# Optimization experiments

Measured on AMD Instinct MI355X. Metric: run time of the kernel, lower is better.

The kernel has to match this reference:

```python
import jax, jax.numpy as jnp
import numpy as np

NUM_HEADS = 16
DIM_HEAD = 64
SCALE = DIM_HEAD ** -0.5


def setup_inputs() -> dict:
    key = jax.random.key(0)
    k1, k2, k3 = jax.random.split(key, 3)
    b, s, h = 2, 2048, 1024
    x = jax.random.normal(k1, (b, s, h), dtype=jnp.float32)
    w_qkv = jax.random.normal(k2, (3 * h, h), dtype=jnp.float32) * (h ** -0.5)
    w_out = jax.random.normal(k3, (h, h), dtype=jnp.float32) * (h ** -0.5)
    b_out = jnp.zeros((h,), dtype=jnp.float32)
    return {"x": x, "w_qkv": w_qkv, "w_out": w_out, "b_out": b_out}


def reference(x, w_qkv, w_out, b_out):
    b, s, hid = x.shape
    # qkv projection (no bias): [b, s, 3*hid]
    qkv = jnp.einsum('bsh,oh->bso', x, w_qkv)
    # split order in original rearrange is (qkv, heads, dim_head)
    qkv = qkv.reshape(b, s, 3, NUM_HEADS, DIM_HEAD)
    q = jnp.transpose(qkv[:, :, 0], (0, 2, 1, 3))  # [b, H, s, d]
    k = jnp.transpose(qkv[:, :, 1], (0, 2, 1, 3))
    v = jnp.transpose(qkv[:, :, 2], (0, 2, 1, 3))
    # naive attention: full [b, H, s, s] score matrix, as in the source
    att = jnp.einsum('bhxd,bhyd->bhxy', q, k) * SCALE
    att = jax.nn.softmax(att, axis=-1)
    out = jnp.einsum('bhxy,bhyd->bhxd', att, v)  # [b, H, s, d]
    out = jnp.transpose(out, (0, 2, 1, 3)).reshape(b, s, NUM_HEADS * DIM_HEAD)
    return jnp.einsum('bsi,oi->bso', out, w_out) + b_out
```

## Files before the change

### kernel.cpp

```cpp
#include <hip/hip_runtime.h>
#include <hip/hip_bf16.h>

#define B_ 2
#define S_ 2048
#define HID 1024
#define NH 16
#define DH 64
#define QKV_N (3*HID)
#define M_ROWS (B_*S_)

typedef __attribute__((ext_vector_type(8))) short short8;
typedef __attribute__((ext_vector_type(4))) short short4v;
typedef __attribute__((ext_vector_type(4))) float floatx4;
typedef unsigned int uint;

#define QSCALE 0.18033688f

__device__ __forceinline__ short8 load8(const __hip_bfloat16* p) {
    return *(const short8*)p;
}

#if __has_builtin(__builtin_amdgcn_exp2f)
#define EXP2F(x) __builtin_amdgcn_exp2f(x)
#else
#define EXP2F(x) exp2f(x)
#endif

__device__ __forceinline__ uint pack_bf16_2(float lo, float hi) {
    uint ul = __float_as_uint(lo) + 0x8000u;
    uint uh = __float_as_uint(hi) + 0x8000u;
    return __builtin_amdgcn_perm(uh, ul, 0x07060302);
}
__device__ __forceinline__ uint pack_bf16_2_rtne(float lo, float hi) {
    uint ul = __float_as_uint(lo); ul += 0x7FFFu + ((ul >> 16) & 1u);
    uint uh = __float_as_uint(hi); uh += 0x7FFFu + ((uh >> 16) & 1u);
    return __builtin_amdgcn_perm(uh, ul, 0x07060302);
}

#define ASYNC16(gptr, lptr) \
    __builtin_amdgcn_global_load_lds((const __attribute__((address_space(1))) void*)(gptr), \
                                     (__attribute__((address_space(3))) void*)(lptr), 16, 0, 0)
#define RAW_BARRIER() asm volatile("s_barrier" ::: "memory")

__global__ __launch_bounds__(256) void cvt_all(
    const float* __restrict__ x, const float* __restrict__ wq,
    const float* __restrict__ wo, __hip_bfloat16* __restrict__ out)
{
    const int n0 = M_ROWS * HID, n1 = QKV_N * HID;
    int i = (blockIdx.x * 256 + threadIdx.x) * 4;
    const float* src; int off;
    if (i < n0)           { src = x;  off = i; }
    else if (i < n0 + n1) { src = wq; off = i - n0; }
    else                  { src = wo; off = i - n0 - n1; }
    float4 v = *(const float4*)(src + off);
    uint2 r;
    r.x = pack_bf16_2_rtne(v.x, v.y);
    r.y = pack_bf16_2_rtne(v.z, v.w);
    *(uint2*)(out + i) = r;
}

#define BK 32
#define NITER 32
template<int MODE, int TMB>
__global__ __launch_bounds__(256, (TMB == 128) ? 3 : 4) void gemm_bt_kernel(
    const __hip_bfloat16* __restrict__ A,
    const __hip_bfloat16* __restrict__ Bw,
    const float* __restrict__ biasf,
    __hip_bfloat16* __restrict__ C,
    float* __restrict__ Cf,
    __hip_bfloat16* __restrict__ VT,
    int Mdim, int Ndim, int Kdim)
{
    constexpr int NI = TMB / 32;
    constexpr int CA = TMB / 64;
    constexpr int WAITG = 0x0F70 | (CA + 2);
    __shared__ alignas(16) __hip_bfloat16 As[3][TMB * BK];
    __shared__ alignas(16) __hip_bfloat16 Bs[3][128 * BK];

    const int tid  = threadIdx.x;
    const int wave = tid >> 6;
    const int lane = tid & 63;
    const int q = lane >> 4;
    const int r = lane & 15;
    const int m_blk = blockIdx.y * TMB;
    const int n_blk = blockIdx.x * 128;
    const int wm = (wave >> 1) * (TMB / 2);
    const int wn = (wave & 1) * 64;

    const __hip_bfloat16* Abase = A + (size_t)m_blk * Kdim;
    const __hip_bfloat16* Bbase = Bw + (size_t)n_blk * Kdim;

    floatx4 acc[NI][4];
#pragma unroll
    for (int i = 0; i < NI; i++)
#pragma unroll
        for (int j = 0; j < 4; j++) acc[i][j] = (floatx4){0.f, 0.f, 0.f, 0.f};

    auto stage = [&](int bf, int kt) {
#pragma unroll
        for (int c = 0; c < CA; c++) {
            int ch = tid + c * 256;
            ASYNC16(Abase + (size_t)(ch >> 2) * Kdim + kt + (ch & 3) * 8, &As[bf][ch * 8]);
        }
#pragma unroll
        for (int c = 0; c < 2; c++) {
            int ch = tid + c * 256;
            ASYNC16(Bbase + (size_t)(ch >> 2) * Kdim + kt + (ch & 3) * 8, &Bs[bf][ch * 8]);
        }
    };
    auto compute = [&](int bf) {
        short8 a[NI], b[4];
#pragma unroll
        for (int i = 0; i < NI; i++) a[i] = *(const short8*)&As[bf][(wm + i * 16 + r) * BK + q * 8];
#pragma unroll
        for (int j = 0; j < 4; j++) b[j] = *(const short8*)&Bs[bf][(wn + j * 16 + r) * BK + q * 8];
#pragma unroll
        for (int i = 0; i < NI; i++)
#pragma unroll
            for (int j = 0; j < 4; j++)
                acc[i][j] = __builtin_amdgcn_mfma_f32_16x16x32_bf16(b[j], a[i], acc[i][j], 0, 0, 0);
    };

    stage(0, 0);
    stage(1, BK);
#pragma unroll 3
    for (int it = 0; it < NITER - 2; it++) {
        __builtin_amdgcn_s_waitcnt(WAITG);
        RAW_BARRIER();
        stage((it + 2) % 3, (it + 2) * BK);
        compute(it % 3);
    }
    __builtin_amdgcn_s_waitcnt(WAITG);
    RAW_BARRIER();
    compute((NITER - 2) % 3);
    __builtin_amdgcn_s_waitcnt(0x0F70);
    RAW_BARRIER();
    compute((NITER - 1) % 3);

#pragma unroll
    for (int i = 0; i < NI; i++) {
        const int m = m_blk + wm + i * 16 + r;
#pragma unroll
        for (int j = 0; j < 4; j++) {
            const int n0 = n_blk + wn + j * 16 + q * 4;
            if (MODE == 2) {
                float4 bv = *(const float4*)&biasf[n0];
                float4 ov;
                ov.x = acc[i][j][0] + bv.x;
                ov.y = acc[i][j][1] + bv.y;
                ov.z = acc[i][j][2] + bv.z;
                ov.w = acc[i][j][3] + bv.w;
                *(float4*)&Cf[(size_t)m * Ndim + n0] = ov;
            } else if (n_blk < 2 * HID) {
                float s = (n0 < HID) ? QSCALE : 1.0f;
                uint2 pk;
                pk.x = pack_bf16_2_rtne(acc[i][j][0] * s, acc[i][j][1] * s);
                pk.y = pack_bf16_2_rtne(acc[i][j][2] * s, acc[i][j][3] * s);
                *(uint2*)&C[(size_t)m * QKV_N + n0] = pk;
            } else {
                int bidx = m >> 11;
                int srow = m & (S_ - 1);
                int c = srow & 31;
                int sp = (srow & ~31) | ((c & 15) << 1) | ((c >> 4) & 1);
#pragma unroll
                for (int reg = 0; reg < 4; reg++) {
                    int dfull = n0 + reg - 2 * HID;
                    VT[((size_t)bidx * HID + dfull) * S_ + sp] =
                        __float2bfloat16(acc[i][j][reg]);
                }
            }
        }
    }
}

#define KT 32
#define PPAD 40

__global__ __launch_bounds__(512, 4) void flash_kernel(
    const __hip_bfloat16* __restrict__ qkv,
    const __hip_bfloat16* __restrict__ VTp,
    __hip_bfloat16* __restrict__ O)
{
    __shared__ alignas(16) char smem[69632];
    __hip_bfloat16* lds_k = (__hip_bfloat16*)smem;
    __hip_bfloat16* lds_v = (__hip_bfloat16*)(smem + 24576);
    __hip_bfloat16* lds_p = (__hip_bfloat16*)(smem + 49152);

    const int tid  = threadIdx.x;
    const int wave = tid >> 6;
    const int lane = tid & 63;
    const int q = lane >> 4;
    const int r = lane & 15;
    const int ww   = wave & 3;
    const int khid = wave >> 2;
    const int bh = blockIdx.x;
    const int b  = bh >> 4;
    const int h  = bh & 15;
    const int s0 = blockIdx.y * 128 + ww * 32;

    const __hip_bfloat16* Qbase = qkv + (size_t)b * S_ * QKV_N + h * DH;
    const __hip_bfloat16* Kbase = Qbase + HID;
    const __hip_bfloat16* Vbase = VTp + ((size_t)b * HID + h * DH) * S_;

    const int sr = ww * 8 + (lane >> 3);
    const int kcg = (lane & 7) ^ ((lane >> 3) & 7);
    const __hip_bfloat16* gK = Kbase + (size_t)(khid * 1024 + sr) * QKV_N + kcg * 8;
    const int kldso = sr * 64 + (lane & 7) * 8;
    const int vr = ww * 16 + (lane >> 2);
    const int fv = (vr + (vr >> 2)) & 3;
    const int vcg = (lane & 3) ^ fv;
    const __hip_bfloat16* gV = Vbase + (size_t)vr * S_ + khid * 1024 + vcg * 8;
    const int vldso = vr * 32 + (lane & 3) * 8;

    auto stage = [&](int bf, int it) {
        ASYNC16(gK + (size_t)(it * KT) * QKV_N, &lds_k[(bf * 2 + khid) * 2048 + kldso]);
        ASYNC16(gV + it * KT,                   &lds_v[(bf * 2 + khid) * 2048 + vldso]);
    };

    floatx4 o_acc[2][4];
    floatx4 l_acc[2];
#pragma unroll
    for (int rt = 0; rt < 2; rt++) {
        l_acc[rt] = (floatx4){0.f, 0.f, 0.f, 0.f};
#pragma unroll
        for (int nb = 0; nb < 4; nb++) o_acc[rt][nb] = (floatx4){0.f, 0.f, 0.f, 0.f};
    }
    short8 ones;
#pragma unroll
    for (int i = 0; i < 8; i++) ones[i] = (short)0x3F80;

    __hip_bfloat16* Pw = &lds_p[wave * 1280];

    short8 a_q[2][2];
    auto compute = [&](int bf) {
        const __hip_bfloat16* Kt = &lds_k[(bf * 2 + khid) * 2048];
        const __hip_bfloat16* Vt = &lds_v[(bf * 2 + khid) * 2048];
        short8 bk[2][2];
#pragma unroll
        for (int ct = 0; ct < 2; ct++)
#pragma unroll
            for (int kh = 0; kh < 2; kh++)
                bk[ct][kh] = *(const short8*)&Kt[(ct * 16 + r) * 64 + ((kh * 4 + q) ^ (r & 7)) * 8];
        short8 vb[4];
#pragma unroll
        for (int nb = 0; nb < 4; nb++) {
            int d = nb * 16 + r;
            vb[nb] = *(const short8*)&Vt[d * 32 + ((q ^ ((d + (d >> 2)) & 3)) * 8)];
        }

        short8 pa[2];
#pragma unroll
        for (int rt = 0; rt < 2; rt++) {
            floatx4 sc[2];
#pragma unroll
            for (int ct = 0; ct < 2; ct++) {
                floatx4 z = (floatx4){0.f, 0.f, 0.f, 0.f};
                z = __builtin_amdgcn_mfma_f32_16x16x32_bf16(a_q[rt][0], bk[ct][0], z, 0, 0, 0);
                z = __builtin_amdgcn_mfma_f32_16x16x32_bf16(a_q[rt][1], bk[ct][1], z, 0, 0, 0);
                sc[ct] = z;
            }
#pragma unroll
            for (int reg = 0; reg < 4; reg++) {
                float e0 = EXP2F(sc[0][reg]);
                float e1 = EXP2F(sc[1][reg]);
                *(uint*)&Pw[(rt * 16 + q * 4 + reg) * PPAD + 2 * r] = pack_bf16_2(e0, e1);
            }
            pa[rt] = *(const short8*)&Pw[(rt * 16 + r) * PPAD + q * 8];
        }

        __builtin_amdgcn_s_setprio(1);
#pragma unroll
        for (int rt = 0; rt < 2; rt++) {
            l_acc[rt] = __builtin_amdgcn_mfma_f32_16x16x32_bf16(pa[rt], ones, l_acc[rt], 0, 0, 0);
#pragma unroll
            for (int nb = 0; nb < 4; nb++)
                o_acc[rt][nb] = __builtin_amdgcn_mfma_f32_16x16x32_bf16(pa[rt], vb[nb], o_acc[rt][nb], 0, 0, 0);
        }
        __builtin_amdgcn_s_setprio(0);
    };

    auto step = [&](int it, int bf) {
        __builtin_amdgcn_s_waitcnt(0x0F72);
        RAW_BARRIER();
        stage((bf + 2) % 3, it + 2);
        compute(bf);
    };

    stage(0, 0);
#pragma unroll
    for (int rt = 0; rt < 2; rt++)
#pragma unroll
        for (int kh = 0; kh < 2; kh++)
            a_q[rt][kh] = load8(Qbase + (size_t)(s0 + rt * 16 + r) * QKV_N + kh * 32 + q * 8);
    __builtin_amdgcn_s_waitcnt(0x0F70);
    stage(1, 1);

    for (int itb = 0; itb < 30; itb += 3) {
        step(itb + 0, 0);
        step(itb + 1, 1);
        step(itb + 2, 2);
    }
    __builtin_amdgcn_s_waitcnt(0x0F72);
    RAW_BARRIER();
    compute(0);
    __builtin_amdgcn_s_waitcnt(0x0F70);
    RAW_BARRIER();
    compute(1);

    __syncthreads();
    float* of = (float*)smem;
    float* lf = (float*)(smem + 32768);
    if (khid == 1) {
#pragma unroll
        for (int rt = 0; rt < 2; rt++) {
#pragma unroll
            for (int nb = 0; nb < 4; nb++)
                *(floatx4*)&of[ww * 2048 + (rt * 4 + nb) * 256 + lane * 4] = o_acc[rt][nb];
            *(floatx4*)&lf[ww * 512 + rt * 256 + lane * 4] = l_acc[rt];
        }
    }
    __syncthreads();
    if (khid == 0) {
#pragma unroll
        for (int rt = 0; rt < 2; rt++) {
            l_acc[rt] += *(const floatx4*)&lf[ww * 512 + rt * 256 + lane * 4];
#pragma unroll
            for (int nb = 0; nb < 4; nb++)
                o_acc[rt][nb] += *(const floatx4*)&of[ww * 2048 + (rt * 4 + nb) * 256 + lane * 4];
        }
#pragma unroll
        for (int rt = 0; rt < 2; rt++) {
#pragma unroll
            for (int reg = 0; reg < 4; reg++) {
                float inv = 1.f / l_acc[rt][reg];
                int srow2 = s0 + rt * 16 + q * 4 + reg;
                __hip_bfloat16* Orow = O + ((size_t)b * S_ + srow2) * HID + h * DH;
#pragma unroll
                for (int nb = 0; nb < 4; nb++)
                    Orow[nb * 16 + r] = __float2bfloat16(o_acc[rt][nb][reg] * inv);
            }
        }
    }
}

extern "C" void kernel_launch(void* const* d_in, const int* in_sizes, int n_in,
                              void* d_out, int out_size, void* d_ws, size_t ws_size,
                              hipStream_t stream) {
    const float* x_f     = (const float*)d_in[0];
    const float* w_qkv_f = (const float*)d_in[1];
    const float* w_out_f = (const float*)d_in[2];
    const float* b_out_f = (const float*)d_in[3];
    float* out = (float*)d_out;

    __hip_bfloat16* xb      = (__hip_bfloat16*)d_ws;
    __hip_bfloat16* wqkvb   = xb    + (size_t)M_ROWS * HID;
    __hip_bfloat16* woutb   = wqkvb + (size_t)QKV_N * HID;
    __hip_bfloat16* qkv_ws  = woutb + (size_t)HID * HID;
    __hip_bfloat16* vt_ws   = qkv_ws + (size_t)M_ROWS * QKV_N;
    __hip_bfloat16* attn_ws = vt_ws + (size_t)B_ * HID * S_;

    dim3 blk(256);
    {
        int ntot = M_ROWS * HID + QKV_N * HID + HID * HID;
        cvt_all<<<dim3(ntot / 1024), blk, 0, stream>>>(x_f, w_qkv_f, w_out_f, xb);
    }

    gemm_bt_kernel<1, 128><<<dim3(QKV_N / 128, M_ROWS / 128), blk, 0, stream>>>(
        xb, wqkvb, nullptr, qkv_ws, nullptr, vt_ws, M_ROWS, QKV_N, HID);
    flash_kernel<<<dim3(B_ * NH, S_ / 128), dim3(512), 0, stream>>>(qkv_ws, vt_ws, attn_ws);
    gemm_bt_kernel<2, 64><<<dim3(HID / 128, M_ROWS / 64), blk, 0, stream>>>(
        attn_ws, woutb, b_out_f, nullptr, out, nullptr, M_ROWS, HID, HID);
}
```

Baseline: 181.0 us.

## Keep softmax probabilities in registers by transposing score MFMA, drop LDS round-trip

Swaps the operand order of the QK^T MFMA so each lane's score accumulator already matches the A-operand layout needed for the PV MFMA, packing exp2 results directly into registers instead of writing P to LDS and reading it back. The V transpose layout written by the QKV GEMM drops its row permutation, and V fragments are now gathered as two 4-element LDS reads to match the new k ordering. This removes the per-wave P scratch in LDS (shrinking shared memory) and its store/load latency, at the cost of more, smaller V reads and a layout change that must stay consistent across both kernels.

Measured after the change: 181.0 us. Within noise of the previous version (-0.0%).

```diff
diff --git a/kernel.cpp b/kernel.cpp
--- a/kernel.cpp
+++ b/kernel.cpp
@@ -12,6 +12,7 @@
 typedef __attribute__((ext_vector_type(8))) short short8;
 typedef __attribute__((ext_vector_type(4))) short short4v;
 typedef __attribute__((ext_vector_type(4))) float floatx4;
+typedef __attribute__((ext_vector_type(4))) unsigned int uint4v;
 typedef unsigned int uint;
 
 #define QSCALE 0.18033688f
@@ -160,12 +161,10 @@
             } else {
                 int bidx = m >> 11;
                 int srow = m & (S_ - 1);
-                int c = srow & 31;
-                int sp = (srow & ~31) | ((c & 15) << 1) | ((c >> 4) & 1);
 #pragma unroll
                 for (int reg = 0; reg < 4; reg++) {
                     int dfull = n0 + reg - 2 * HID;
-                    VT[((size_t)bidx * HID + dfull) * S_ + sp] =
+                    VT[((size_t)bidx * HID + dfull) * S_ + srow] =
                         __float2bfloat16(acc[i][j][reg]);
                 }
             }
@@ -174,17 +173,15 @@
 }
 
 #define KT 32
-#define PPAD 40
 
 __global__ __launch_bounds__(512, 4) void flash_kernel(
     const __hip_bfloat16* __restrict__ qkv,
     const __hip_bfloat16* __restrict__ VTp,
     __hip_bfloat16* __restrict__ O)
 {
-    __shared__ alignas(16) char smem[69632];
+    __shared__ alignas(16) char smem[49152];
     __hip_bfloat16* lds_k = (__hip_bfloat16*)smem;
     __hip_bfloat16* lds_v = (__hip_bfloat16*)(smem + 24576);
-    __hip_bfloat16* lds_p = (__hip_bfloat16*)(smem + 49152);
 
     const int tid  = threadIdx.x;
     const int wave = tid >> 6;
@@ -229,8 +226,6 @@
 #pragma unroll
     for (int i = 0; i < 8; i++) ones[i] = (short)0x3F80;
 
-    __hip_bfloat16* Pw = &lds_p[wave * 1280];
-
     short8 a_q[2][2];
     auto compute = [&](int bf) {
         const __hip_bfloat16* Kt = &lds_k[(bf * 2 + khid) * 2048];
@@ -245,38 +240,36 @@
 #pragma unroll
         for (int nb = 0; nb < 4; nb++) {
             int d = nb * 16 + r;
-            vb[nb] = *(const short8*)&Vt[d * 32 + ((q ^ ((d + (d >> 2)) & 3)) * 8)];
-        }
-
-        short8 pa[2];
+            int fvd = (d + (d >> 2)) & 3;
+            short4v lo = *(const short4v*)&Vt[d * 32 + (((q >> 1) ^ fvd) * 8 + (q & 1) * 4)];
+            short4v hi = *(const short4v*)&Vt[d * 32 + ((((q >> 1) + 2) ^ fvd) * 8 + (q & 1) * 4)];
+            vb[nb] = __builtin_shufflevector(lo, hi, 0, 1, 2, 3, 4, 5, 6, 7);
+        }
+
 #pragma unroll
         for (int rt = 0; rt < 2; rt++) {
             floatx4 sc[2];
 #pragma unroll
             for (int ct = 0; ct < 2; ct++) {
                 floatx4 z = (floatx4){0.f, 0.f, 0.f, 0.f};
-                z = __builtin_amdgcn_mfma_f32_16x16x32_bf16(a_q[rt][0], bk[ct][0], z, 0, 0, 0);
-                z = __builtin_amdgcn_mfma_f32_16x16x32_bf16(a_q[rt][1], bk[ct][1], z, 0, 0, 0);
+                z = __builtin_amdgcn_mfma_f32_16x16x32_bf16(bk[ct][0], a_q[rt][0], z, 0, 0, 0);
+                z = __builtin_amdgcn_mfma_f32_16x16x32_bf16(bk[ct][1], a_q[rt][1], z, 0, 0, 0);
                 sc[ct] = z;
             }
-#pragma unroll
-            for (int reg = 0; reg < 4; reg++) {
-                float e0 = EXP2F(sc[0][reg]);
-                float e1 = EXP2F(sc[1][reg]);
-                *(uint*)&Pw[(rt * 16 + q * 4 + reg) * PPAD + 2 * r] = pack_bf16_2(e0, e1);
-            }
-            pa[rt] = *(const short8*)&Pw[(rt * 16 + r) * PPAD + q * 8];
-        }
-
-        __builtin_amdgcn_s_setprio(1);
-#pragma unroll
-        for (int rt = 0; rt < 2; rt++) {
-            l_acc[rt] = __builtin_amdgcn_mfma_f32_16x16x32_bf16(pa[rt], ones, l_acc[rt], 0, 0, 0);
+            uint4v up;
+            up.x = pack_bf16_2(EXP2F(sc[0][0]), EXP2F(sc[0][1]));
+            up.y = pack_bf16_2(EXP2F(sc[0][2]), EXP2F(sc[0][3]));
+            up.z = pack_bf16_2(EXP2F(sc[1][0]), EXP2F(sc[1][1]));
+            up.w = pack_bf16_2(EXP2F(sc[1][2]), EXP2F(sc[1][3]));
+            short8 pa = __builtin_bit_cast(short8, up);
+
+            __builtin_amdgcn_s_setprio(1);
+            l_acc[rt] = __builtin_amdgcn_mfma_f32_16x16x32_bf16(pa, ones, l_acc[rt], 0, 0, 0);
 #pragma unroll
             for (int nb = 0; nb < 4; nb++)
-                o_acc[rt][nb] = __builtin_amdgcn_mfma_f32_16x16x32_bf16(pa[rt], vb[nb], o_acc[rt][nb], 0, 0, 0);
-        }
-        __builtin_amdgcn_s_setprio(0);
+                o_acc[rt][nb] = __builtin_amdgcn_mfma_f32_16x16x32_bf16(pa, vb[nb], o_acc[rt][nb], 0, 0, 0);
+            __builtin_amdgcn_s_setprio(0);
+        }
     };
 
     auto step = [&](int it, int bf) {
```
